# Kernel tuning notes

Hardware: AMD Instinct MI355X
Metric: run time of the kernel (lower is better)

## Reference

```python
import jax, jax.numpy as jnp
import numpy as np

NUM_HEADS = 16
EMBED_DIM = 1024
B, L = 1, 4096


def setup_inputs() -> dict:
    key = jax.random.key(0)
    k1, k2, k3 = jax.random.split(key, 3)
    x = jax.random.normal(k1, (B, L, EMBED_DIM), dtype=jnp.float32)
    # torch nn.Linear weights are [out_features, in_features]
    w_attn = jax.random.normal(k2, (3 * EMBED_DIM, EMBED_DIM), dtype=jnp.float32) * (EMBED_DIM ** -0.5)
    w_proj = jax.random.normal(k3, (EMBED_DIM, EMBED_DIM), dtype=jnp.float32) * (EMBED_DIM ** -0.5)
    return {"x": x, "w_attn": w_attn, "w_proj": w_proj}


def reference(x, w_attn, w_proj):
    b, l, e = x.shape
    h = NUM_HEADS
    hd = e // h
    qkv = x @ w_attn.T                      # [B, L, 3E]
    q, k, v = jnp.split(qkv, 3, axis=-1)
    # [B, H, L, hd]
    q = q.reshape(b, l, h, hd).transpose(0, 2, 1, 3)
    k = k.reshape(b, l, h, hd).transpose(0, 2, 1, 3)
    v = v.reshape(b, l, h, hd).transpose(0, 2, 1, 3)
    scale = 1.0 / jnp.sqrt(jnp.asarray(hd, dtype=x.dtype))
    scores = jnp.einsum('bhld,bhsd->bhls', q, k) * scale  # [B, H, L, L]
    causal = jnp.tril(jnp.ones((l, l), dtype=bool))
    scores = jnp.where(causal, scores, jnp.asarray(-jnp.inf, dtype=scores.dtype))
    attn = jax.nn.softmax(scores, axis=-1)
    y = jnp.einsum('bhls,bhsd->bhld', attn, v)            # [B, H, L, hd]
    y = y.transpose(0, 2, 1, 3).reshape(b, l, e)
    return y @ w_proj.T
```

## Files before the change

kernel.cpp:

```cpp
#include <hip/hip_runtime.h>

#define LSEQ 4096
#define EMB  1024
#define NH   16
#define HD   64

typedef __attribute__((ext_vector_type(8)))  __bf16 bf16x8;
typedef __attribute__((ext_vector_type(4)))  float f32x4;
typedef __attribute__((ext_vector_type(16))) float f32x16;
typedef __attribute__((ext_vector_type(8)))  unsigned short u16x8;
typedef __attribute__((ext_vector_type(4)))  unsigned short u16x4;
typedef __attribute__((ext_vector_type(4)))  unsigned int u32x4;

__device__ __forceinline__ unsigned short f2bf(float f) {
    union { float f; unsigned u; } v; v.f = f;
    unsigned r = v.u + 0x7fffu + ((v.u >> 16) & 1u);
    return (unsigned short)(r >> 16);
}

__device__ __forceinline__ unsigned cvt_pk_bf16(float a, float b) {
    unsigned r;
    asm("v_cvt_pk_bf16_f32 %0, %1, %2" : "=v"(r) : "v"(a), "v"(b));
    return r;
}

__device__ __forceinline__ void plswap(unsigned &x, unsigned &y) {
    asm volatile("v_permlane32_swap_b32 %0, %1" : "+v"(x), "+v"(y));
}

__device__ __forceinline__ f32x4 mfma16(u16x8 a, u16x8 b, f32x4 c) {
    return __builtin_amdgcn_mfma_f32_16x16x32_bf16(
        __builtin_bit_cast(bf16x8, a), __builtin_bit_cast(bf16x8, b), c, 0, 0, 0);
}

__device__ __forceinline__ f32x16 mfma32(u16x8 a, u16x8 b, f32x16 c) {
    return __builtin_amdgcn_mfma_f32_32x32x16_bf16(
        __builtin_bit_cast(bf16x8, a), __builtin_bit_cast(bf16x8, b), c, 0, 0, 0);
}

__device__ __forceinline__ void gload16(const void* g, void* l) {
    __builtin_amdgcn_global_load_lds((const __attribute__((address_space(1))) unsigned int*)g,
                                     (__attribute__((address_space(3))) unsigned int*)l,
                                     16, 0, 0);
}

#define NXC (LSEQ * EMB / 4)
#define NAC (3 * EMB * EMB / 4)
#define NPC (EMB * EMB / 4)
__global__ __launch_bounds__(256) void cvt_all(const float* __restrict__ x,
                                               const float* __restrict__ wa,
                                               const float* __restrict__ wp,
                                               unsigned short* __restrict__ out) {
    int i = blockIdx.x * 256 + threadIdx.x;
    if (i >= NXC + NAC + NPC) return;
    const float* src;
    if (i < NXC)             src = x + (size_t)i * 4;
    else if (i < NXC + NAC)  src = wa + (size_t)(i - NXC) * 4;
    else                     src = wp + (size_t)(i - NXC - NAC) * 4;
    f32x4 v = *(const f32x4*)src;
    u16x4 o;
    o[0] = f2bf(v[0]); o[1] = f2bf(v[1]); o[2] = f2bf(v[2]); o[3] = f2bf(v[3]);
    *(u16x4*)(out + (size_t)i * 4) = o;
}

__global__ __launch_bounds__(256, 2) void gemm_qkv(const unsigned short* __restrict__ A,
                                                   const unsigned short* __restrict__ B,
                                                   unsigned short* __restrict__ Qo,
                                                   unsigned short* __restrict__ Ko,
                                                   unsigned short* __restrict__ Vto) {
    __shared__ unsigned short As[128 * 32];
    __shared__ unsigned short Bs[128 * 32];
    const int tid = threadIdx.x;
    const int lane = tid & 63;
    const int wv = tid >> 6;
    const int wm = wv >> 1, wn = wv & 1;
    const int li = lane & 15, g = lane >> 4;
    const int m0 = blockIdx.y * 128, n0 = blockIdx.x * 128;
    f32x4 acc[4][4] = {};
    for (int k0 = 0; k0 < EMB; k0 += 32) {
        #pragma unroll
        for (int c = 0; c < 2; ++c) {
            const int o = c * 4096 + tid * 16;
            const int r = o >> 6, cb = o & 63;
            gload16((const char*)A + ((size_t)(m0 + r) * EMB + k0) * 2 + cb, (char*)As + o);
            gload16((const char*)B + ((size_t)(n0 + r) * EMB + k0) * 2 + cb, (char*)Bs + o);
        }
        __syncthreads();
        u16x8 af[4], bfr[4];
        #pragma unroll
        for (int mb = 0; mb < 4; ++mb)
            af[mb] = *(const u16x8*)(As + (wm * 64 + mb * 16 + li) * 32 + g * 8);
        #pragma unroll
        for (int nb = 0; nb < 4; ++nb)
            bfr[nb] = *(const u16x8*)(Bs + (wn * 64 + nb * 16 + li) * 32 + g * 8);
        #pragma unroll
        for (int mb = 0; mb < 4; ++mb)
            #pragma unroll
            for (int nb = 0; nb < 4; ++nb)
                acc[mb][nb] = mfma16(af[mb], bfr[nb], acc[mb][nb]);
        __syncthreads();
    }
    for (int mb = 0; mb < 4; ++mb) {
        for (int nb = 0; nb < 4; ++nb) {
            for (int r = 0; r < 4; ++r) {
                const int m = m0 + wm * 64 + mb * 16 + g * 4 + r;
                const int n = n0 + wn * 64 + nb * 16 + li;
                const float v = acc[mb][nb][r];
                if (n < EMB) {
                    Qo[((size_t)(n >> 6) * LSEQ + m) * HD + (n & 63)] = f2bf(v * 0.1803368801111244f);
                } else if (n < 2 * EMB) {
                    const int c = n - EMB;
                    Ko[((size_t)(c >> 6) * LSEQ + m) * HD + (c & 63)] = f2bf(v);
                } else {
                    const int c = n - 2 * EMB;
                    Vto[((size_t)(c >> 6) * HD + (c & 63)) * LSEQ + m] = f2bf(v);
                }
            }
        }
    }
}

__global__ __launch_bounds__(512, 4) void attn_fwd(const unsigned short* __restrict__ Q,
                                                   const unsigned short* __restrict__ K,
                                                   const unsigned short* __restrict__ Vt,
                                                   unsigned short* __restrict__ Y) {
    __shared__ char LB[2][32768];
    const int d0 = blockIdx.x;
    const int grp = d0 & 255;
    const int head = 2 * (grp & 7) + ((grp >> 3) & 1);
    const int t16 = grp >> 4;
    const int s = (d0 < 256) ? (31 - t16) : t16;
    const int tid = threadIdx.x, lane = tid & 63, w = tid >> 6;
    const int qs = w & 3, par = w >> 2;
    const int li = lane & 31, hf = lane >> 5;
    const int qw0 = s * 128 + qs * 32;
    const int qrow = qw0 + li;
    const int jmaxw = 2 * s + (qs >> 1);
    const int nst = s + 1;
    const char* KhB = (const char*)(K + (size_t)head * LSEQ * HD);
    const char* VhB = (const char*)(Vt + (size_t)head * HD * LSEQ);

    u16x8 bq[4];
    #pragma unroll
    for (int ks = 0; ks < 4; ++ks)
        bq[ks] = *(const u16x8*)(Q + ((size_t)head * LSEQ + qrow) * HD + ks * 16 + hf * 8);

    int off[4];
    #pragma unroll
    for (int ks = 0; ks < 4; ++ks) {
        const int c = 2 * ks + hf;
        off[ks] = c * 1024 + (((li & 24) | ((li & 7) ^ c)) << 4);
    }

    const int row0 = (tid >> 3) & 31, sch = tid & 7, half = tid >> 8;
    const int wd0 = sch * 1024 + (((row0 & 24) | ((row0 & 7) ^ sch)) << 4);

    u16x8 kr0, kr1, vr0, vr1;
    #define LOADKV(js_) do {                                                              \
        const char* kp_ = KhB + ((size_t)((js_) * 128 + half * 64 + row0)) * 128 + sch * 16; \
        const char* vp_ = VhB + (size_t)row0 * (LSEQ * 2) + ((js_) * 128 + half * 64) * 2 + sch * 16; \
        kr0 = *(const u16x8*)kp_;                                                         \
        kr1 = *(const u16x8*)(kp_ + 32 * 128);                                            \
        vr0 = *(const u16x8*)vp_;                                                         \
        vr1 = *(const u16x8*)(vp_ + (size_t)32 * (LSEQ * 2));                             \
    } while (0)
    #define WRITEKV(b_) do {                                                              \
        char* base_ = LB[b_] + half * 8192;                                               \
        *(u16x8*)(base_ + wd0)               = kr0;                                       \
        *(u16x8*)(base_ + wd0 + 512)         = kr1;                                       \
        *(u16x8*)(base_ + 16384 + wd0)       = vr0;                                       \
        *(u16x8*)(base_ + 16384 + wd0 + 512) = vr1;                                       \
    } while (0)

    float l_i = 0.f;
    f32x16 oA = {}, oB = {};

    LOADKV(0);
    WRITEKV(0);
    __syncthreads();
    for (int js = 0; js < nst; ++js) {
        const int cur = js & 1;
        if (js + 1 < nst) LOADKV(js + 1);
        const int j = 2 * js + par;
        if (j <= jmaxw) {
            const char* Kb = LB[cur] + par * 8192;
            const char* Vb = LB[cur] + 16384 + par * 8192;
            f32x16 sA = {}, sB = {};
            __builtin_amdgcn_s_setprio(1);
            #pragma unroll
            for (int ks = 0; ks < 4; ++ks) {
                const u16x8 ka0 = *(const u16x8*)(Kb + off[ks]);
                const u16x8 ka1 = *(const u16x8*)(Kb + off[ks] + 512);
                sA = mfma32(ka0, bq[ks], sA);
                sB = mfma32(ka1, bq[ks], sB);
            }
            __builtin_amdgcn_s_setprio(0);
            if (j == jmaxw && (j * 64 + 63 > qw0)) {
                const int kbase = j * 64;
                #pragma unroll
                for (int r = 0; r < 16; ++r) {
                    const int kvl = kbase + (r & 3) + 8 * (r >> 2) + 4 * hf;
                    if (kvl > qrow)      sA[r] = -1e30f;
                    if (kvl + 32 > qrow) sB[r] = -1e30f;
                }
            }
            float s0 = 0.f, s1 = 0.f;
            unsigned uA[8], uB[8];
            #pragma unroll
            for (int wd = 0; wd < 8; ++wd) {
                const float a0 = __builtin_amdgcn_exp2f(sA[2 * wd]);
                const float a1 = __builtin_amdgcn_exp2f(sA[2 * wd + 1]);
                const float b0 = __builtin_amdgcn_exp2f(sB[2 * wd]);
                const float b1 = __builtin_amdgcn_exp2f(sB[2 * wd + 1]);
                s0 += a0 + a1; s1 += b0 + b1;
                uA[wd] = cvt_pk_bf16(a0, a1);
                uB[wd] = cvt_pk_bf16(b0, b1);
            }
            l_i += s0 + s1;
            plswap(uA[0], uA[2]); plswap(uA[1], uA[3]);
            plswap(uA[4], uA[6]); plswap(uA[5], uA[7]);
            plswap(uB[0], uB[2]); plswap(uB[1], uB[3]);
            plswap(uB[4], uB[6]); plswap(uB[5], uB[7]);
            const u32x4 wA0 = {uA[0], uA[1], uA[2], uA[3]};
            const u32x4 wA1 = {uA[4], uA[5], uA[6], uA[7]};
            const u32x4 wB0 = {uB[0], uB[1], uB[2], uB[3]};
            const u32x4 wB1 = {uB[4], uB[5], uB[6], uB[7]};
            const u16x8 ap0 = __builtin_bit_cast(u16x8, wA0);
            const u16x8 ap1 = __builtin_bit_cast(u16x8, wA1);
            const u16x8 ap2 = __builtin_bit_cast(u16x8, wB0);
            const u16x8 ap3 = __builtin_bit_cast(u16x8, wB1);
            const u16x8 va0 = *(const u16x8*)(Vb + off[0]);
            const u16x8 va1 = *(const u16x8*)(Vb + off[1]);
            const u16x8 va2 = *(const u16x8*)(Vb + off[2]);
            const u16x8 va3 = *(const u16x8*)(Vb + off[3]);
            const u16x8 vc0 = *(const u16x8*)(Vb + off[0] + 512);
            const u16x8 vc1 = *(const u16x8*)(Vb + off[1] + 512);
            const u16x8 vc2 = *(const u16x8*)(Vb + off[2] + 512);
            const u16x8 vc3 = *(const u16x8*)(Vb + off[3] + 512);
            __builtin_amdgcn_s_setprio(1);
            oA = mfma32(ap0, va0, oA);
            oA = mfma32(ap1, va1, oA);
            oA = mfma32(ap2, va2, oA);
            oA = mfma32(ap3, va3, oA);
            oB = mfma32(ap0, vc0, oB);
            oB = mfma32(ap1, vc1, oB);
            oB = mfma32(ap2, vc2, oB);
            oB = mfma32(ap3, vc3, oB);
            __builtin_amdgcn_s_setprio(0);
        }
        if (js + 1 < nst) WRITEKV(cur ^ 1);
        __syncthreads();
    }
    #undef LOADKV
    #undef WRITEKV
    if (par == 1) {
        float* po = (float*)(LB[0] + qs * 8192);
        #pragma unroll
        for (int r = 0; r < 16; ++r) {
            po[r * 64 + lane]        = oA[r];
            po[(16 + r) * 64 + lane] = oB[r];
        }
        ((float*)LB[1])[qs * 64 + lane] = l_i;
    }
    __syncthreads();
    if (par == 0) {
        const float* po = (const float*)(LB[0] + qs * 8192);
        l_i += ((const float*)LB[1])[qs * 64 + lane];
        #pragma unroll
        for (int r = 0; r < 16; ++r) {
            oA[r] += po[r * 64 + lane];
            oB[r] += po[(16 + r) * 64 + lane];
        }
        const float lt = l_i + __shfl_xor(l_i, 32);
        const float linv = 1.0f / lt;
        #pragma unroll
        for (int r = 0; r < 16; ++r) {
            const int ql = (r & 3) + 8 * (r >> 2) + 4 * hf;
            const float gl = __shfl(linv, ql);
            Y[(size_t)(qw0 + ql) * EMB + head * HD + li]      = f2bf(oA[r] * gl);
            Y[(size_t)(qw0 + ql) * EMB + head * HD + 32 + li] = f2bf(oB[r] * gl);
        }
    }
}

__global__ __launch_bounds__(256, 2) void gemm_proj(const unsigned short* __restrict__ A,
                                                    const unsigned short* __restrict__ B,
                                                    float* __restrict__ C) {
    __shared__ unsigned short As[128 * 32];
    __shared__ unsigned short Bs[128 * 32];
    const int tid = threadIdx.x;
    const int lane = tid & 63;
    const int wv = tid >> 6;
    const int wm = wv >> 1, wn = wv & 1;
    const int li = lane & 15, g = lane >> 4;
    const int m0 = blockIdx.y * 128, n0 = blockIdx.x * 128;
    f32x4 acc[4][4] = {};
    for (int k0 = 0; k0 < EMB; k0 += 32) {
        #pragma unroll
        for (int c = 0; c < 2; ++c) {
            const int o = c * 4096 + tid * 16;
            const int r = o >> 6, cb = o & 63;
            gload16((const char*)A + ((size_t)(m0 + r) * EMB + k0) * 2 + cb, (char*)As + o);
            gload16((const char*)B + ((size_t)(n0 + r) * EMB + k0) * 2 + cb, (char*)Bs + o);
        }
        __syncthreads();
        u16x8 af[4], bfr[4];
        #pragma unroll
        for (int mb = 0; mb < 4; ++mb)
            af[mb] = *(const u16x8*)(As + (wm * 64 + mb * 16 + li) * 32 + g * 8);
        #pragma unroll
        for (int nb = 0; nb < 4; ++nb)
            bfr[nb] = *(const u16x8*)(Bs + (wn * 64 + nb * 16 + li) * 32 + g * 8);
        #pragma unroll
        for (int mb = 0; mb < 4; ++mb)
            #pragma unroll
            for (int nb = 0; nb < 4; ++nb)
                acc[mb][nb] = mfma16(af[mb], bfr[nb], acc[mb][nb]);
        __syncthreads();
    }
    for (int mb = 0; mb < 4; ++mb)
        for (int nb = 0; nb < 4; ++nb)
            for (int r = 0; r < 4; ++r) {
                const int m = m0 + wm * 64 + mb * 16 + g * 4 + r;
                const int n = n0 + wn * 64 + nb * 16 + li;
                C[(size_t)m * EMB + n] = acc[mb][nb][r];
            }
}

extern "C" void kernel_launch(void* const* d_in, const int* in_sizes, int n_in,
                              void* d_out, int out_size, void* d_ws, size_t ws_size,
                              hipStream_t stream) {
    const float* x      = (const float*)d_in[0];
    const float* w_attn = (const float*)d_in[1];
    const float* w_proj = (const float*)d_in[2];
    float* out = (float*)d_out;

    unsigned short* ws  = (unsigned short*)d_ws;
    unsigned short* xb  = ws;
    unsigned short* wab = xb + (size_t)LSEQ * EMB;
    unsigned short* wpb = wab + (size_t)3 * EMB * EMB;
    unsigned short* Qb  = wpb + (size_t)EMB * EMB;
    unsigned short* Kb  = Qb + (size_t)LSEQ * EMB;
    unsigned short* Vtb = Kb + (size_t)LSEQ * EMB;
    unsigned short* Yb  = Vtb + (size_t)LSEQ * EMB;

    const int ntot = NXC + NAC + NPC;
    cvt_all<<<(ntot + 255) / 256, 256, 0, stream>>>(x, w_attn, w_proj, xb);
    gemm_qkv<<<dim3(3 * EMB / 128, LSEQ / 128), 256, 0, stream>>>(xb, wab, Qb, Kb, Vtb);
    attn_fwd<<<dim3(512), 512, 0, stream>>>(Qb, Kb, Vtb, Yb);
    gemm_proj<<<dim3(EMB / 128, LSEQ / 128), 256, 0, stream>>>(Yb, wpb, out);
}
```

Measured before the change: 126.2 us.

## Deepen GEMM K-tile to 64 with XOR-swizzled LDS, XCD-aware block remap, vectorized V store

Both GEMMs now stage a K-step of 64 instead of 32, halving the number of barrier pairs per tile. The shared-memory layout gets an XOR swizzle on 16-byte chunks to avoid bank conflicts. The grids are flattened and block indices remapped so consecutive blocks on each XCD share tiles for L2 locality. The QKV epilogue branches once per block and writes V transposed with 4-element vector stores. Doubling LDS per block may reduce occupancy.

After: 114.4 us. 1.1x faster.

```diff
diff --git a/kernel.cpp b/kernel.cpp
--- a/kernel.cpp
+++ b/kernel.cpp
@@ -68,55 +68,83 @@
                                                    unsigned short* __restrict__ Qo,
                                                    unsigned short* __restrict__ Ko,
                                                    unsigned short* __restrict__ Vto) {
-    __shared__ unsigned short As[128 * 32];
-    __shared__ unsigned short Bs[128 * 32];
+    __shared__ unsigned short As[128 * 64];
+    __shared__ unsigned short Bs[128 * 64];
+    const int d0 = blockIdx.x;
+    const int wg = (d0 & 7) * 96 + (d0 >> 3);
+    const int bx = wg % 24, by = wg / 24;
     const int tid = threadIdx.x;
     const int lane = tid & 63;
     const int wv = tid >> 6;
     const int wm = wv >> 1, wn = wv & 1;
     const int li = lane & 15, g = lane >> 4;
-    const int m0 = blockIdx.y * 128, n0 = blockIdx.x * 128;
+    const int m0 = by * 128, n0 = bx * 128;
     f32x4 acc[4][4] = {};
-    for (int k0 = 0; k0 < EMB; k0 += 32) {
-        #pragma unroll
-        for (int c = 0; c < 2; ++c) {
-            const int o = c * 4096 + tid * 16;
-            const int r = o >> 6, cb = o & 63;
-            gload16((const char*)A + ((size_t)(m0 + r) * EMB + k0) * 2 + cb, (char*)As + o);
-            gload16((const char*)B + ((size_t)(n0 + r) * EMB + k0) * 2 + cb, (char*)Bs + o);
-        }
-        __syncthreads();
-        u16x8 af[4], bfr[4];
-        #pragma unroll
+    for (int k0 = 0; k0 < EMB; k0 += 64) {
+        #pragma unroll
+        for (int i = 0; i < 4; ++i) {
+            const int o = i * 4096 + tid * 16;
+            const int r = o >> 7;
+            const int sl = (o >> 4) & 7;
+            const int sc = (sl ^ (r & 7)) << 4;
+            gload16((const char*)A + ((size_t)(m0 + r) * EMB + k0) * 2 + sc, (char*)As + o);
+            gload16((const char*)B + ((size_t)(n0 + r) * EMB + k0) * 2 + sc, (char*)Bs + o);
+        }
+        __syncthreads();
+        u16x8 af[2][4], bfr[2][4];
+        #pragma unroll
+        for (int h = 0; h < 2; ++h) {
+            #pragma unroll
+            for (int mb = 0; mb < 4; ++mb) {
+                const int row = wm * 64 + mb * 16 + li;
+                const int c = h * 4 + g;
+                af[h][mb] = *(const u16x8*)((const char*)As + row * 128 + (((c ^ (row & 7))) << 4));
+            }
+            #pragma unroll
+            for (int nb = 0; nb < 4; ++nb) {
+                const int row = wn * 64 + nb * 16 + li;
+                const int c = h * 4 + g;
+                bfr[h][nb] = *(const u16x8*)((const char*)Bs + row * 128 + (((c ^ (row & 7))) << 4));
+            }
+        }
+        #pragma unroll
+        for (int h = 0; h < 2; ++h)
+            #pragma unroll
+            for (int mb = 0; mb < 4; ++mb)
+                #pragma unroll
+                for (int nb = 0; nb < 4; ++nb)
+                    acc[mb][nb] = mfma16(af[h][mb], bfr[h][nb], acc[mb][nb]);
+        __syncthreads();
+    }
+    if (n0 < EMB) {
         for (int mb = 0; mb < 4; ++mb)
-            af[mb] = *(const u16x8*)(As + (wm * 64 + mb * 16 + li) * 32 + g * 8);
-        #pragma unroll
-        for (int nb = 0; nb < 4; ++nb)
-            bfr[nb] = *(const u16x8*)(Bs + (wn * 64 + nb * 16 + li) * 32 + g * 8);
-        #pragma unroll
+            for (int nb = 0; nb < 4; ++nb)
+                for (int r = 0; r < 4; ++r) {
+                    const int m = m0 + wm * 64 + mb * 16 + g * 4 + r;
+                    const int n = n0 + wn * 64 + nb * 16 + li;
+                    Qo[((size_t)(n >> 6) * LSEQ + m) * HD + (n & 63)] =
+                        f2bf(acc[mb][nb][r] * 0.1803368801111244f);
+                }
+    } else if (n0 < 2 * EMB) {
         for (int mb = 0; mb < 4; ++mb)
-            #pragma unroll
             for (int nb = 0; nb < 4; ++nb)
-                acc[mb][nb] = mfma16(af[mb], bfr[nb], acc[mb][nb]);
-        __syncthreads();
-    }
-    for (int mb = 0; mb < 4; ++mb) {
-        for (int nb = 0; nb < 4; ++nb) {
-            for (int r = 0; r < 4; ++r) {
-                const int m = m0 + wm * 64 + mb * 16 + g * 4 + r;
-                const int n = n0 + wn * 64 + nb * 16 + li;
-                const float v = acc[mb][nb][r];
-                if (n < EMB) {
-                    Qo[((size_t)(n >> 6) * LSEQ + m) * HD + (n & 63)] = f2bf(v * 0.1803368801111244f);
-                } else if (n < 2 * EMB) {
-                    const int c = n - EMB;
-                    Ko[((size_t)(c >> 6) * LSEQ + m) * HD + (c & 63)] = f2bf(v);
-                } else {
-                    const int c = n - 2 * EMB;
-                    Vto[((size_t)(c >> 6) * HD + (c & 63)) * LSEQ + m] = f2bf(v);
+                for (int r = 0; r < 4; ++r) {
+                    const int m = m0 + wm * 64 + mb * 16 + g * 4 + r;
+                    const int c = n0 - EMB + wn * 64 + nb * 16 + li;
+                    Ko[((size_t)(c >> 6) * LSEQ + m) * HD + (c & 63)] = f2bf(acc[mb][nb][r]);
                 }
-            }
-        }
+    } else {
+        for (int mb = 0; mb < 4; ++mb)
+            for (int nb = 0; nb < 4; ++nb) {
+                const int mbase = m0 + wm * 64 + mb * 16 + g * 4;
+                const int c = n0 - 2 * EMB + wn * 64 + nb * 16 + li;
+                u16x4 pv;
+                pv[0] = f2bf(acc[mb][nb][0]);
+                pv[1] = f2bf(acc[mb][nb][1]);
+                pv[2] = f2bf(acc[mb][nb][2]);
+                pv[3] = f2bf(acc[mb][nb][3]);
+                *(u16x4*)(Vto + ((size_t)(c >> 6) * HD + (c & 63)) * LSEQ + mbase) = pv;
+            }
     }
 }
 
@@ -286,36 +314,52 @@
 __global__ __launch_bounds__(256, 2) void gemm_proj(const unsigned short* __restrict__ A,
                                                     const unsigned short* __restrict__ B,
                                                     float* __restrict__ C) {
-    __shared__ unsigned short As[128 * 32];
-    __shared__ unsigned short Bs[128 * 32];
+    __shared__ unsigned short As[128 * 64];
+    __shared__ unsigned short Bs[128 * 64];
+    const int d0 = blockIdx.x;
+    const int wg = (d0 & 7) * 32 + (d0 >> 3);
+    const int bx = wg % 8, by = wg / 8;
     const int tid = threadIdx.x;
     const int lane = tid & 63;
     const int wv = tid >> 6;
     const int wm = wv >> 1, wn = wv & 1;
     const int li = lane & 15, g = lane >> 4;
-    const int m0 = blockIdx.y * 128, n0 = blockIdx.x * 128;
+    const int m0 = by * 128, n0 = bx * 128;
     f32x4 acc[4][4] = {};
-    for (int k0 = 0; k0 < EMB; k0 += 32) {
-        #pragma unroll
-        for (int c = 0; c < 2; ++c) {
-            const int o = c * 4096 + tid * 16;
-            const int r = o >> 6, cb = o & 63;
-            gload16((const char*)A + ((size_t)(m0 + r) * EMB + k0) * 2 + cb, (char*)As + o);
-            gload16((const char*)B + ((size_t)(n0 + r) * EMB + k0) * 2 + cb, (char*)Bs + o);
-        }
-        __syncthreads();
-        u16x8 af[4], bfr[4];
-        #pragma unroll
-        for (int mb = 0; mb < 4; ++mb)
-            af[mb] = *(const u16x8*)(As + (wm * 64 + mb * 16 + li) * 32 + g * 8);
-        #pragma unroll
-        for (int nb = 0; nb < 4; ++nb)
-            bfr[nb] = *(const u16x8*)(Bs + (wn * 64 + nb * 16 + li) * 32 + g * 8);
-        #pragma unroll
-        for (int mb = 0; mb < 4; ++mb)
-            #pragma unroll
-            for (int nb = 0; nb < 4; ++nb)
-                acc[mb][nb] = mfma16(af[mb], bfr[nb], acc[mb][nb]);
+    for (int k0 = 0; k0 < EMB; k0 += 64) {
+        #pragma unroll
+        for (int i = 0; i < 4; ++i) {
+            const int o = i * 4096 + tid * 16;
+            const int r = o >> 7;
+            const int sl = (o >> 4) & 7;
+            const int sc = (sl ^ (r & 7)) << 4;
+            gload16((const char*)A + ((size_t)(m0 + r) * EMB + k0) * 2 + sc, (char*)As + o);
+            gload16((const char*)B + ((size_t)(n0 + r) * EMB + k0) * 2 + sc, (char*)Bs + o);
+        }
+        __syncthreads();
+        u16x8 af[2][4], bfr[2][4];
+        #pragma unroll
+        for (int h = 0; h < 2; ++h) {
+            #pragma unroll
+            for (int mb = 0; mb < 4; ++mb) {
+                const int row = wm * 64 + mb * 16 + li;
+                const int c = h * 4 + g;
+                af[h][mb] = *(const u16x8*)((const char*)As + row * 128 + (((c ^ (row & 7))) << 4));
+            }
+            #pragma unroll
+            for (int nb = 0; nb < 4; ++nb) {
+                const int row = wn * 64 + nb * 16 + li;
+                const int c = h * 4 + g;
+                bfr[h][nb] = *(const u16x8*)((const char*)Bs + row * 128 + (((c ^ (row & 7))) << 4));
+            }
+        }
+        #pragma unroll
+        for (int h = 0; h < 2; ++h)
+            #pragma unroll
+            for (int mb = 0; mb < 4; ++mb)
+                #pragma unroll
+                for (int nb = 0; nb < 4; ++nb)
+                    acc[mb][nb] = mfma16(af[h][mb], bfr[h][nb], acc[mb][nb]);
         __syncthreads();
     }
     for (int mb = 0; mb < 4; ++mb)
@@ -346,7 +390,7 @@
 
     const int ntot = NXC + NAC + NPC;
     cvt_all<<<(ntot + 255) / 256, 256, 0, stream>>>(x, w_attn, w_proj, xb);
-    gemm_qkv<<<dim3(3 * EMB / 128, LSEQ / 128), 256, 0, stream>>>(xb, wab, Qb, Kb, Vtb);
+    gemm_qkv<<<dim3(768), 256, 0, stream>>>(xb, wab, Qb, Kb, Vtb);
     attn_fwd<<<dim3(512), 512, 0, stream>>>(Qb, Kb, Vtb, Yb);
-    gemm_proj<<<dim3(EMB / 128, LSEQ / 128), 256, 0, stream>>>(Yb, wpb, out);
-}
+    gemm_proj<<<dim3(256), 256, 0, stream>>>(Yb, wpb, out);
+}
```
